# Performance work log

Measured on AMD Instinct MI355X. Metric: run time of the kernel, lower is better.

The kernel has to match this reference:

```python
import jax, jax.numpy as jnp
import numpy as np
import math

N, C_IN, H, W = 8, 256, 64, 64
C_ATT, C_OUT = 128, 256
BN_EPS = 1e-5


def conv_bn_relu(x, w, gamma, beta, mean, var):
    # 1x1 conv (no bias) + BatchNorm (eval mode) + ReLU
    y = jnp.einsum('oc,nchw->nohw', w, x)
    inv = gamma / jnp.sqrt(var + BN_EPS)
    y = y * inv[None, :, None, None] + (beta - mean * inv)[None, :, None, None]
    return jax.nn.relu(y)


def setup_inputs() -> dict:
    key = jax.random.key(0)
    ks = jax.random.split(key, 12)
    x = jax.random.normal(ks[0], (N, C_IN, H, W), dtype=jnp.float32)
    mask = jnp.ones((N, 1, H, W), dtype=jnp.float32)
    reduc_w = jax.random.normal(ks[1], (C_OUT, C_IN), dtype=jnp.float32) * (1.0 / math.sqrt(C_IN))
    reduc_gamma = jnp.ones((C_OUT,), dtype=jnp.float32)
    reduc_beta = jnp.zeros((C_OUT,), dtype=jnp.float32)
    reduc_mean = jax.random.normal(ks[2], (C_OUT,), dtype=jnp.float32) * 0.1
    reduc_var = jax.random.uniform(ks[3], (C_OUT,), dtype=jnp.float32) + 0.5
    att_w = jax.random.normal(ks[4], (C_ATT, C_IN), dtype=jnp.float32) * (1.0 / math.sqrt(C_IN))
    att_gamma = jnp.ones((C_ATT,), dtype=jnp.float32)
    att_beta = jnp.zeros((C_ATT,), dtype=jnp.float32)
    att_mean = jax.random.normal(ks[5], (C_ATT,), dtype=jnp.float32) * 0.1
    att_var = jax.random.uniform(ks[6], (C_ATT,), dtype=jnp.float32) + 0.5
    return {
        'x': x, 'mask': mask,
        'reduc_w': reduc_w, 'reduc_gamma': reduc_gamma, 'reduc_beta': reduc_beta,
        'reduc_mean': reduc_mean, 'reduc_var': reduc_var,
        'att_w': att_w, 'att_gamma': att_gamma, 'att_beta': att_beta,
        'att_mean': att_mean, 'att_var': att_var,
    }


def reference(x, mask, reduc_w, reduc_gamma, reduc_beta, reduc_mean, reduc_var,
              att_w, att_gamma, att_beta, att_mean, att_var):
    n, _, h, w = x.shape
    x_feat = conv_bn_relu(x, reduc_w, reduc_gamma, reduc_beta, reduc_mean, reduc_var)   # [n,C_OUT,h,w]
    x_atten = conv_bn_relu(x, att_w, att_gamma, att_beta, att_mean, att_var)            # [n,C_ATT,h,w]
    c = x_atten.shape[1]
    q = x_atten.reshape(n, c, h * w)                                                    # [n,c,HW]
    # energy[n,i,j] = sum_c q[n,c,i]*q[n,c,j] / (1e-8 + sqrt(c))
    energy = jnp.einsum('nci,ncj->nij', q, q) / (1e-8 + math.sqrt(c))
    energy = energy + (mask.reshape(n, 1, h * w) - 1.0) * 1e8
    weight = jax.nn.softmax(energy, axis=2)                                             # [n,HW,HW]
    feat = x_feat.reshape(n, x_feat.shape[1], h * w)                                    # [n,C_OUT,HW]
    out = jnp.einsum('nij,ncj->nci', weight, feat)                                      # [n,C_OUT,HW]
    out = out.reshape(n, feat.shape[1], h, w)
    out = out * mask
    return out
```

## Files before the change

### kernel.cpp

```cpp
#include <hip/hip_runtime.h>
#include <cstdint>
#include <cstddef>

#define NB 8
#define CIN 256
#define HWX 4096
#define CF 256
#define CA 128
#define CT 384

typedef __attribute__((ext_vector_type(8))) _Float16 half8;
typedef __attribute__((ext_vector_type(8))) short short8;
typedef __attribute__((ext_vector_type(4))) float f32x4;
typedef __attribute__((ext_vector_type(4))) unsigned int u32x4;
typedef __attribute__((ext_vector_type(2))) unsigned int u32x2;

#define OFF_WH   0
#define OFF_BIAS (CT*CIN*2)
#define OFF_FEAT (OFF_BIAS + CT*4)
#define OFF_Q    (OFF_FEAT + NB*CF*HWX*2)
#define OFF_NORM (OFF_Q + NB*HWX*CA*2)
#define OFF_G    (OFF_NORM + NB*HWX*4)

__device__ inline unsigned short f16_bits(float f) {
  _Float16 h = (_Float16)f;
  return __builtin_bit_cast(unsigned short, h);
}
__device__ inline half8 ld_half8(const unsigned short* p) {
  short8 r = *(const short8*)p;
  return __builtin_bit_cast(half8, r);
}

__device__ inline void g2l16(const void* g, void* l) {
  __builtin_amdgcn_global_load_lds(
      (const __attribute__((address_space(1))) unsigned int*)g,
      (__attribute__((address_space(3))) unsigned int*)l, 16, 0, 0);
}

__global__ __launch_bounds__(256) void fold_bn_k(
    const float* __restrict__ rw, const float* __restrict__ rg,
    const float* __restrict__ rb, const float* __restrict__ rm, const float* __restrict__ rv,
    const float* __restrict__ aw, const float* __restrict__ ag,
    const float* __restrict__ ab2, const float* __restrict__ am, const float* __restrict__ av,
    unsigned short* __restrict__ wh, float* __restrict__ bias, unsigned* __restrict__ Gmax) {
  int o = blockIdx.x, k = threadIdx.x;
  if (o == 0 && k < NB) Gmax[k] = 0u;
  const float* wsrc; float g, b, m, v;
  if (o < CF) { wsrc = rw + (size_t)o*CIN; g = rg[o]; b = rb[o]; m = rm[o]; v = rv[o]; }
  else { int oa = o - CF; wsrc = aw + (size_t)oa*CIN; g = ag[oa]; b = ab2[oa]; m = am[oa]; v = av[oa]; }
  float inv = g / sqrtf(v + 1e-5f);
  wh[(size_t)o*CIN + k] = f16_bits(wsrc[k] * inv);
  if (k == 0) bias[o] = b - m*inv;
}

__global__ __launch_bounds__(512, 4) void conv_k(
    const float* __restrict__ x, const unsigned short* __restrict__ wh,
    const float* __restrict__ bias, unsigned short* __restrict__ feat,
    unsigned short* __restrict__ q, float* __restrict__ normq,
    unsigned* __restrict__ Gmax) {
  __shared__ unsigned short sX[64*256];
  unsigned short (*sQr)[136] = (unsigned short(*)[136])sX;
  int b = blockIdx.x;
  int n = b & 7, pt0 = b >> 3;
  int p0 = pt0 * 64;
  int t = threadIdx.x;
  int w = t >> 6, lane = t & 63, quad = lane >> 4, col = lane & 15;
  const float* xn = x + (size_t)n*CIN*HWX;

  #pragma unroll
  for (int pass=0; pass<4; pass++) {
    int idx = pass*512 + t;
    int kp = idx >> 4, c4 = idx & 15;
    f32x4 a = *(const f32x4*)(xn + (size_t)(2*kp)*HWX + p0 + c4*4);
    f32x4 c = *(const f32x4*)(xn + (size_t)(2*kp+1)*HWX + p0 + c4*4);
    int unit = kp >> 2, off = kp & 3;
    #pragma unroll
    for (int j=0;j<4;j++) {
      int pos = c4*4 + j;
      unsigned dd = (unsigned)f16_bits(a[j]) | ((unsigned)f16_bits(c[j]) << 16);
      *(unsigned*)&sX[pos*256 + ((unit ^ (pos & 31)) << 3) + off*2] = dd;
    }
  }
  __syncthreads();

  f32x4 fzero = {0.f,0.f,0.f,0.f};
  f32x4 acc[4][3];
  #pragma unroll
  for (int pt=0;pt<4;pt++)
    #pragma unroll
    for (int ot=0;ot<3;ot++) acc[pt][ot] = fzero;

  int ocb = w*48;
  #pragma unroll
  for (int ks=0; ks<8; ks++) {
    half8 B3[3];
    #pragma unroll
    for (int ot=0;ot<3;ot++)
      B3[ot] = ld_half8(wh + (size_t)(ocb + ot*16 + col)*CIN + ks*32 + quad*8);
    half8 A4[4];
    #pragma unroll
    for (int pt=0;pt<4;pt++) {
      int pos = pt*16 + col;
      A4[pt] = ld_half8(&sX[pos*256 + (((ks*4 + quad) ^ (pos & 31)) << 3)]);
    }
    #pragma unroll
    for (int pt=0;pt<4;pt++)
      #pragma unroll
      for (int ot=0;ot<3;ot++)
        acc[pt][ot] = __builtin_amdgcn_mfma_f32_16x16x32_f16(A4[pt], B3[ot], acc[pt][ot], 0, 0, 0);
  }
  __syncthreads();

  float bv[3];
  #pragma unroll
  for (int ot=0;ot<3;ot++) bv[ot] = bias[ocb + ot*16 + col];
  #pragma unroll
  for (int pt=0;pt<4;pt++)
    #pragma unroll
    for (int ot=0;ot<3;ot++) {
      int oc = ocb + ot*16 + col;
      alignas(8) unsigned short u4[4];
      #pragma unroll
      for (int r=0;r<4;r++)
        u4[r] = f16_bits(fmaxf(acc[pt][ot][r] + bv[ot], 0.f));
      if (oc < CF) {
        *(u32x2*)(feat + (size_t)n*CF*HWX + (size_t)oc*HWX + p0 + pt*16 + quad*4) =
            *(const u32x2*)u4;
      } else {
        int cc = oc - CF;
        #pragma unroll
        for (int r=0;r<4;r++)
          sQr[pt*16 + quad*4 + r][cc] = u4[r];
      }
    }
  __syncthreads();

  if (t < 256) {
    int pos = t >> 2, seg = t & 3;
    const unsigned short* src = &sQr[pos][seg*32];
    unsigned short* dst = q + ((size_t)n*HWX + p0 + pos)*CA + seg*32;
    float s2 = 0.f;
    #pragma unroll
    for (int u=0;u<4;u++) {
      short8 v = *(const short8*)(src + u*8);
      *(short8*)(dst + u*8) = v;
      half8 h = __builtin_bit_cast(half8, v);
      #pragma unroll
      for (int e=0;e<8;e++) { float fe = (float)h[e]; s2 += fe*fe; }
    }
    s2 += __shfl_xor(s2, 1, 64);
    s2 += __shfl_xor(s2, 2, 64);
    if (seg == 0) normq[(size_t)n*HWX + p0 + pos] = sqrtf(s2);
    float mx = s2;
    mx = fmaxf(mx, __shfl_xor(mx, 4, 64));
    mx = fmaxf(mx, __shfl_xor(mx, 8, 64));
    mx = fmaxf(mx, __shfl_xor(mx, 16, 64));
    mx = fmaxf(mx, __shfl_xor(mx, 32, 64));
    if (lane == 0) atomicMax(Gmax + n, __float_as_uint(sqrtf(mx)));
  }
}

__global__ __launch_bounds__(512, 4) void flash_k(
    const unsigned short* __restrict__ q, const unsigned short* __restrict__ feat,
    const float* __restrict__ mask, const float* __restrict__ normq,
    const unsigned* __restrict__ Gmax, float* __restrict__ out) {
  __shared__ alignas(16) unsigned short sQ[128*128];
  __shared__ alignas(16) unsigned short sP[64][136];
  __shared__ float sM[128];
  __shared__ float sL[2][64];
  int b = blockIdx.x;
  int n = b & 7, it = b >> 3;
  int i0 = it * 64;
  int t = threadIdx.x;
  int w = t >> 6, lane = t & 63, quad = lane >> 4, col = lane & 15;
  int wq = w & 3, wh = w >> 2;
  const unsigned short* q_n = q + (size_t)n*HWX*CA;
  const unsigned short* f_n = feat + (size_t)n*CF*HWX;
  const float* m_n = mask + (size_t)n*HWX;
  const int rloc = t >> 4 & 31, oct16 = t & 15;
  const float inv_s = 1.0f/(1e-8f + sqrtf(128.0f));

  auto stage_Q = [&](int j0) {
    #pragma unroll
    for (int c=0;c<4;c++) {
      int row = c*32 + rloc;
      int og = oct16 ^ (row & 15);
      g2l16(q_n + (size_t)(j0+row)*CA + og*8, &sQ[(size_t)row*128 + oct16*8]);
    }
    if (t < 32) g2l16(m_n + j0 + t*4, &sM[t*4]);
  };

  half8 ah[4];
  {
    int arow = i0 + wq*16 + col;
    #pragma unroll
    for (int ks=0; ks<4; ks++)
      ah[ks] = ld_half8(q_n + (size_t)arow*CA + ks*32 + quad*8);
  }
  float Gn = __uint_as_float(Gmax[n]);
  float cvals[4];
  #pragma unroll
  for (int r=0;r<4;r++)
    cvals[r] = normq[(size_t)n*HWX + i0 + wq*16 + quad*4 + r] * Gn * inv_s - 5.0f;

  f32x4 fzero = {0.f,0.f,0.f,0.f};
  f32x4 o[4][2];
  #pragma unroll
  for (int ig=0;ig<4;ig++) { o[ig][0] = fzero; o[ig][1] = fzero; }
  float lrun[4] = {0.f,0.f,0.f,0.f};

  stage_Q(0);
  #pragma unroll 1
  for (int ji = 0; ji < 32; ji++) {
    int j0 = ji*128;
    __syncthreads();

    half8 bF01[2][2];
    #pragma unroll
    for (int ks2=0;ks2<2;ks2++)
      #pragma unroll
      for (int ct=0;ct<2;ct++) {
        int c = w*32 + ct*16 + col;
        bF01[ks2][ct] = ld_half8(f_n + (size_t)c*HWX + j0 + ks2*32 + quad*8);
      }

    f32x4 s[4];
    #pragma unroll
    for (int jt=0;jt<4;jt++) s[jt] = fzero;
    #pragma unroll
    for (int jt=0;jt<4;jt++) {
      int rowj = wh*64 + jt*16 + col;
      #pragma unroll
      for (int ks=0; ks<4; ks++) {
        int slot = (ks*4 + quad) ^ (rowj & 15);
        half8 bq = ld_half8(&sQ[rowj*128 + slot*8]);
        s[jt] = __builtin_amdgcn_mfma_f32_16x16x32_f16(ah[ks], bq, s[jt], 0, 0, 0);
      }
    }

    #pragma unroll
    for (int jt=0;jt<4;jt++) {
      float mj = (sM[wh*64 + jt*16 + col] - 1.f) * 1e8f;
      #pragma unroll
      for (int r=0;r<4;r++) {
        float p = __expf(s[jt][r]*inv_s + mj - cvals[r]);
        lrun[r] += p;
        sP[wq*16 + quad*4 + r][wh*64 + jt*16 + col] = f16_bits(p);
      }
    }

    __syncthreads();
    if (ji + 1 < 32) stage_Q(j0+128);

    half8 bF23[2][2];
    #pragma unroll
    for (int ks2=0;ks2<2;ks2++)
      #pragma unroll
      for (int ct=0;ct<2;ct++) {
        int c = w*32 + ct*16 + col;
        bF23[ks2][ct] = ld_half8(f_n + (size_t)c*HWX + j0 + (ks2+2)*32 + quad*8);
      }
    #pragma unroll
    for (int ks2=0; ks2<4; ks2++) {
      half8 aP[4];
      #pragma unroll
      for (int ig=0;ig<4;ig++)
        aP[ig] = ld_half8(&sP[ig*16 + col][ks2*32 + quad*8]);
      #pragma unroll
      for (int ct=0;ct<2;ct++) {
        half8 bF = (ks2 < 2) ? bF01[ks2][ct] : bF23[ks2-2][ct];
        #pragma unroll
        for (int ig=0;ig<4;ig++)
          o[ig][ct] = __builtin_amdgcn_mfma_f32_16x16x32_f16(aP[ig], bF, o[ig][ct], 0, 0, 0);
      }
    }
  }

  #pragma unroll
  for (int r=0;r<4;r++) {
    float ss = lrun[r];
    ss += __shfl_xor(ss, 1, 64);
    ss += __shfl_xor(ss, 2, 64);
    ss += __shfl_xor(ss, 4, 64);
    ss += __shfl_xor(ss, 8, 64);
    lrun[r] = ss;
  }
  #pragma unroll
  for (int r=0;r<4;r++)
    if (col == 0) sL[wh][wq*16 + quad*4 + r] = lrun[r];
  __syncthreads();
  #pragma unroll
  for (int ig=0;ig<4;ig++) {
    int base = ig*16 + quad*4;
    f32x4 l0 = *(const f32x4*)&sL[0][base];
    f32x4 l1 = *(const f32x4*)&sL[1][base];
    f32x4 mv = *(const f32x4*)(m_n + i0 + base);
    f32x4 minv;
    #pragma unroll
    for (int r=0;r<4;r++) minv[r] = mv[r] / (l0[r] + l1[r]);
    #pragma unroll
    for (int ct=0;ct<2;ct++) {
      int c = w*32 + ct*16 + col;
      f32x4 v;
      #pragma unroll
      for (int r=0;r<4;r++) v[r] = o[ig][ct][r] * minv[r];
      *(f32x4*)(out + ((size_t)n*CF + c)*HWX + i0 + base) = v;
    }
  }
}

extern "C" void kernel_launch(void* const* d_in, const int* in_sizes, int n_in,
                              void* d_out, int out_size, void* d_ws, size_t ws_size,
                              hipStream_t stream) {
  const float* x    = (const float*)d_in[0];
  const float* mask = (const float*)d_in[1];
  const float* rw   = (const float*)d_in[2];
  const float* rg   = (const float*)d_in[3];
  const float* rb   = (const float*)d_in[4];
  const float* rm   = (const float*)d_in[5];
  const float* rv   = (const float*)d_in[6];
  const float* aw   = (const float*)d_in[7];
  const float* ag   = (const float*)d_in[8];
  const float* ab   = (const float*)d_in[9];
  const float* am   = (const float*)d_in[10];
  const float* av   = (const float*)d_in[11];
  float* out = (float*)d_out;
  char* ws = (char*)d_ws;
  unsigned short* wh = (unsigned short*)(ws + OFF_WH);
  float* bias = (float*)(ws + OFF_BIAS);
  unsigned short* feat = (unsigned short*)(ws + OFF_FEAT);
  unsigned short* q    = (unsigned short*)(ws + OFF_Q);
  float* normq = (float*)(ws + OFF_NORM);
  unsigned* Gmax = (unsigned*)(ws + OFF_G);

  hipLaunchKernelGGL(fold_bn_k, dim3(CT), dim3(CIN), 0, stream,
                     rw, rg, rb, rm, rv, aw, ag, ab, am, av, wh, bias, Gmax);
  hipLaunchKernelGGL(conv_k, dim3(512), dim3(512), 0, stream,
                     x, wh, bias, feat, q, normq, Gmax);
  hipLaunchKernelGGL(flash_k, dim3(512), dim3(512), 0, stream,
                     q, feat, mask, normq, Gmax, out);
}
```

Before: 293.9 us.

## Load Q directly from global, double-buffer P tile, drop one barrier per iteration

Removes the shared-memory staging of Q key tiles and the mask, so each wave reads its Q B-operands and mask values straight from global memory (relying on L1/L2 caching). The P tile in LDS is now double-buffered by iteration parity, which allows dropping the barrier at the top of the loop, leaving one barrier per iteration. P rows are padded to 132 halves, which breaks 16-byte alignment, so P reads are split into two 8-byte loads. In exchange, global/cache traffic for Q grows because the Q tile is no longer shared across waves through LDS, and an extra barrier is added before the final sL write.

Measured after the change: 487.2 us. 65.8% more time.

```diff
diff --git a/kernel.cpp b/kernel.cpp
--- a/kernel.cpp
+++ b/kernel.cpp
@@ -11,6 +11,7 @@
 
 typedef __attribute__((ext_vector_type(8))) _Float16 half8;
 typedef __attribute__((ext_vector_type(8))) short short8;
+typedef __attribute__((ext_vector_type(4))) short s16x4;
 typedef __attribute__((ext_vector_type(4))) float f32x4;
 typedef __attribute__((ext_vector_type(4))) unsigned int u32x4;
 typedef __attribute__((ext_vector_type(2))) unsigned int u32x2;
@@ -164,9 +165,7 @@
     const unsigned short* __restrict__ q, const unsigned short* __restrict__ feat,
     const float* __restrict__ mask, const float* __restrict__ normq,
     const unsigned* __restrict__ Gmax, float* __restrict__ out) {
-  __shared__ alignas(16) unsigned short sQ[128*128];
-  __shared__ alignas(16) unsigned short sP[64][136];
-  __shared__ float sM[128];
+  __shared__ alignas(16) unsigned short sP[2][64][132];
   __shared__ float sL[2][64];
   int b = blockIdx.x;
   int n = b & 7, it = b >> 3;
@@ -177,18 +176,7 @@
   const unsigned short* q_n = q + (size_t)n*HWX*CA;
   const unsigned short* f_n = feat + (size_t)n*CF*HWX;
   const float* m_n = mask + (size_t)n*HWX;
-  const int rloc = t >> 4 & 31, oct16 = t & 15;
   const float inv_s = 1.0f/(1e-8f + sqrtf(128.0f));
-
-  auto stage_Q = [&](int j0) {
-    #pragma unroll
-    for (int c=0;c<4;c++) {
-      int row = c*32 + rloc;
-      int og = oct16 ^ (row & 15);
-      g2l16(q_n + (size_t)(j0+row)*CA + og*8, &sQ[(size_t)row*128 + oct16*8]);
-    }
-    if (t < 32) g2l16(m_n + j0 + t*4, &sM[t*4]);
-  };
 
   half8 ah[4];
   {
@@ -209,11 +197,24 @@
   for (int ig=0;ig<4;ig++) { o[ig][0] = fzero; o[ig][1] = fzero; }
   float lrun[4] = {0.f,0.f,0.f,0.f};
 
-  stage_Q(0);
   #pragma unroll 1
   for (int ji = 0; ji < 32; ji++) {
     int j0 = ji*128;
-    __syncthreads();
+    unsigned short (*sPc)[132] = sP[ji & 1];
+
+    f32x4 s[4];
+    #pragma unroll
+    for (int jt=0;jt<4;jt++) s[jt] = fzero;
+    #pragma unroll
+    for (int jt=0;jt<4;jt++) {
+      int rowj = j0 + wh*64 + jt*16 + col;
+      const unsigned short* qr = q_n + (size_t)rowj*CA + quad*8;
+      #pragma unroll
+      for (int ks=0; ks<4; ks++) {
+        half8 bq = ld_half8(qr + ks*32);
+        s[jt] = __builtin_amdgcn_mfma_f32_16x16x32_f16(ah[ks], bq, s[jt], 0, 0, 0);
+      }
+    }
 
     half8 bF01[2][2];
     #pragma unroll
@@ -224,33 +225,18 @@
         bF01[ks2][ct] = ld_half8(f_n + (size_t)c*HWX + j0 + ks2*32 + quad*8);
       }
 
-    f32x4 s[4];
-    #pragma unroll
-    for (int jt=0;jt<4;jt++) s[jt] = fzero;
     #pragma unroll
     for (int jt=0;jt<4;jt++) {
-      int rowj = wh*64 + jt*16 + col;
-      #pragma unroll
-      for (int ks=0; ks<4; ks++) {
-        int slot = (ks*4 + quad) ^ (rowj & 15);
-        half8 bq = ld_half8(&sQ[rowj*128 + slot*8]);
-        s[jt] = __builtin_amdgcn_mfma_f32_16x16x32_f16(ah[ks], bq, s[jt], 0, 0, 0);
-      }
-    }
-
-    #pragma unroll
-    for (int jt=0;jt<4;jt++) {
-      float mj = (sM[wh*64 + jt*16 + col] - 1.f) * 1e8f;
+      float mj = (m_n[j0 + wh*64 + jt*16 + col] - 1.f) * 1e8f;
       #pragma unroll
       for (int r=0;r<4;r++) {
         float p = __expf(s[jt][r]*inv_s + mj - cvals[r]);
         lrun[r] += p;
-        sP[wq*16 + quad*4 + r][wh*64 + jt*16 + col] = f16_bits(p);
+        sPc[wq*16 + quad*4 + r][wh*64 + jt*16 + col] = f16_bits(p);
       }
     }
 
     __syncthreads();
-    if (ji + 1 < 32) stage_Q(j0+128);
 
     half8 bF23[2][2];
     #pragma unroll
@@ -264,8 +250,13 @@
     for (int ks2=0; ks2<4; ks2++) {
       half8 aP[4];
       #pragma unroll
-      for (int ig=0;ig<4;ig++)
-        aP[ig] = ld_half8(&sP[ig*16 + col][ks2*32 + quad*8]);
+      for (int ig=0;ig<4;ig++) {
+        const unsigned short* pp = &sPc[ig*16 + col][ks2*32 + quad*8];
+        s16x4 lo = *(const s16x4*)pp;
+        s16x4 hi = *(const s16x4*)(pp + 4);
+        short8 vv = __builtin_shufflevector(lo, hi, 0,1,2,3,4,5,6,7);
+        aP[ig] = __builtin_bit_cast(half8, vv);
+      }
       #pragma unroll
       for (int ct=0;ct<2;ct++) {
         half8 bF = (ks2 < 2) ? bF01[ks2][ct] : bF23[ks2-2][ct];
@@ -285,6 +276,7 @@
     ss += __shfl_xor(ss, 8, 64);
     lrun[r] = ss;
   }
+  __syncthreads();
   #pragma unroll
   for (int r=0;r<4;r++)
     if (col == 0) sL[wh][wq*16 + quad*4 + r] = lrun[r];
```
